# Optimization experiments

Measured on AMD Instinct MI355X. Metric: run time of the kernel, lower is better.

## Reference

```python
import jax, jax.numpy as jnp
import numpy as np

EPS = 1e-12  # tf.nn.l2_normalize epsilon


def setup_inputs() -> dict:
    key = jax.random.key(0)
    k1, k2, k3 = jax.random.split(key, 3)
    T, NC, FW = 16384, 2048, 100
    x = jax.random.normal(k1, (T, NC), dtype=jnp.float32)
    weights = jax.random.normal(k2, (FW, NC), dtype=jnp.float32)
    biases = jax.random.normal(k3, (1, NC), dtype=jnp.float32)
    return {"x": x, "weights": weights, "biases": biases}


def reference(x, weights, biases):
    # x: [T, NC] (batch_size is the time axis), weights: [FW, NC], biases: [1, NC]
    FW, NC = weights.shape
    # pos_constraint then L2-normalize each filter along the lag axis
    w = jnp.maximum(weights, 0.0)
    w = w * jax.lax.rsqrt(jnp.maximum(jnp.sum(w * w, axis=0, keepdims=True), EPS))
    # The original pads the filter with FW trailing zeros and runs a SAME conv2d
    # over a [NC, T, 1, 1] input, then takes diag_part to recover the per-channel
    # result. With kernel size 2*FW, SAME pads (FW-1) above / FW below; the FW
    # trailing zero taps never contribute, so this equals a cross-correlation
    # with left padding FW-1: out[t, c] = sum_k w[k, c] * x[t + k - (FW-1), c].
    xT = x.T[None]                 # [1, NC, T]
    kern = w.T[:, None, :]         # [NC, 1, FW] depthwise kernel (OIH)
    pre = jax.lax.conv_general_dilated(
        xT, kern,
        window_strides=(1,),
        padding=[(FW - 1, 0)],
        dimension_numbers=("NCH", "OIH", "NCH"),
        feature_group_count=NC,
    )                              # [1, NC, T]
    pre = pre[0].T + biases        # [T, NC]
    return pre  # activation_func='lin' -> identity
```

## Files before the change

### kernel.cpp

```cpp
#include <hip/hip_runtime.h>


#define T_TOT 16384
#define NCH   2048
#define FW    100
#define CB    32
#define TB    128
#define NTHR  256
#define TTH   16
#define ROWL  292
#define WROW  108
#define NSEG  12
#define NCHUNK_TOT (T_TOT / TB)

#define KC_PHASE(PH, NS) do {                                                   \
    int ro_ = tk & 255;                                                         \
    float4 n0_ = *(const float4*)(rrow + ro_);                                  \
    float4 n1_ = *(const float4*)(rrow + ro_ + 4);                              \
    float4 w0_ = *(const float4*)(wp);                                          \
    float4 w1_ = *(const float4*)(wp + 4);                                      \
    float wk_[8];                                                               \
    wk_[0]=w0_.x; wk_[1]=w0_.y; wk_[2]=w0_.z; wk_[3]=w0_.w;                     \
    wk_[4]=w1_.x; wk_[5]=w1_.y; wk_[6]=w1_.z; wk_[7]=w1_.w;                     \
    xw[(NS)+0]=n0_.x; xw[(NS)+1]=n0_.y; xw[(NS)+2]=n0_.z; xw[(NS)+3]=n0_.w;     \
    xw[(NS)+4]=n1_.x; xw[(NS)+5]=n1_.y; xw[(NS)+6]=n1_.z; xw[(NS)+7]=n1_.w;     \
    _Pragma("unroll")                                                           \
    for (int u_ = 0; u_ < 8; ++u_) {                                            \
      _Pragma("unroll")                                                         \
      for (int i_ = 0; i_ < 16; ++i_)                                           \
        acc[i_] = fmaf(wk_[u_], xw[((PH) + u_ + i_) % 24], acc[i_]);            \
    }                                                                           \
    tk += 8; wp += 8;                                                           \
} while (0)

__global__ __launch_bounds__(NTHR)
void catent_fir(const float* __restrict__ x,
                const float* __restrict__ wraw,
                const float* __restrict__ bias,
                float* __restrict__ out) {
    __shared__ float ring[CB * ROWL];
    __shared__ float wl[CB * WROW];
    __shared__ float scl[CB];

    const int tid   = threadIdx.x;
    const int cgrp  = blockIdx.x & 63;
    const int sidx  = blockIdx.x >> 6;
    const int cbase = cgrp * CB;

    const int ch0 = (sidx * NCHUNK_TOT) / NSEG;
    const int ch1 = ((sidx + 1) * NCHUNK_TOT) / NSEG;
    const int tseg0 = ch0 * TB;

    const int c = tid & 31;
    const int g = tid >> 5;

    for (int i = tid; i < FW * CB; i += NTHR) {
        int k = i >> 5, cc = i & 31;
        wl[cc * WROW + k + 1] = fmaxf(wraw[(size_t)k * NCH + cbase + cc], 0.0f);
    }
    if (tid < CB) {
        wl[tid * WROW + 0] = 0.0f;
        for (int j = FW + 1; j < WROW; ++j) wl[tid * WROW + j] = 0.0f;
    }
    __syncthreads();
    if (tid < CB) {
        float s = 0.0f;
        #pragma unroll 4
        for (int k = 1; k <= FW; ++k) { float v = wl[tid * WROW + k]; s = fmaf(v, v, s); }
        scl[tid] = rsqrtf(fmaxf(s, 1e-12f));
    }
    __syncthreads();
    for (int i = tid; i < FW * CB; i += NTHR) {
        int k = i >> 5, cc = i & 31;
        wl[cc * WROW + k + 1] *= scl[cc];
    }

    {
        float* rw = &ring[c * ROWL];
        for (int p = 0; p < 2; ++p) {
            int tbase = tseg0 - TB + p * TB + g * 16;
            float v[16];
            #pragma unroll
            for (int j = 0; j < 16; ++j) {
                int t = tbase + j;
                v[j] = (t >= 0) ? x[(size_t)t * NCH + cbase + c] : 0.0f;
            }
            int rm = tbase & 255;
            #pragma unroll
            for (int q = 0; q < 4; ++q)
                *(float4*)(rw + rm + q * 4) = make_float4(v[q*4], v[q*4+1], v[q*4+2], v[q*4+3]);
            if (rm < 32) {
                #pragma unroll
                for (int q = 0; q < 4; ++q)
                    *(float4*)(rw + 256 + rm + q * 4) = make_float4(v[q*4], v[q*4+1], v[q*4+2], v[q*4+3]);
            }
        }
    }
    __syncthreads();

    const float biasr = bias[cbase + c];
    const float* rrow = &ring[c * ROWL];
    const float* wrow = &wl[c * WROW];
    float* rwr = &ring[c * ROWL];

    for (int ch = ch0; ch < ch1; ++ch) {
        const int t0 = ch * TB;
        const bool do_stage = (ch + 1 < ch1);

        float stv[16];
        if (do_stage) {
            const size_t gb = (size_t)(t0 + TB + g * 16) * NCH + cbase + c;
            #pragma unroll
            for (int j = 0; j < 16; ++j) stv[j] = x[gb + (size_t)j * NCH];
        }

        float acc[16];
        #pragma unroll
        for (int i = 0; i < 16; ++i) acc[i] = biasr;

        float xw[24];
        const int base0 = t0 + g * 16 - 100;

        {
            int ro = base0 & 255;
            #pragma unroll
            for (int q = 0; q < 6; ++q) {
                float4 v = *(const float4*)(rrow + ro + q * 4);
                xw[q*4+0] = v.x; xw[q*4+1] = v.y; xw[q*4+2] = v.z; xw[q*4+3] = v.w;
            }
            float4 w0 = *(const float4*)(wrow);
            float4 w1 = *(const float4*)(wrow + 4);
            float wk[8];
            wk[0]=w0.x; wk[1]=w0.y; wk[2]=w0.z; wk[3]=w0.w;
            wk[4]=w1.x; wk[5]=w1.y; wk[6]=w1.z; wk[7]=w1.w;
            #pragma unroll
            for (int u = 0; u < 8; ++u) {
                #pragma unroll
                for (int i = 0; i < 16; ++i)
                    acc[i] = fmaf(wk[u], xw[(u + i) % 24], acc[i]);
            }
        }

        int tk = base0 + 24;
        const float* wp = wrow + 8;
        #pragma unroll 1
        for (int m = 0; m < 4; ++m) {
            KC_PHASE(8, 0);
            KC_PHASE(16, 8);
            KC_PHASE(0, 16);
        }

        __syncthreads();

        if (do_stage) {
            int rm = (t0 + TB + g * 16) & 255;
            #pragma unroll
            for (int q = 0; q < 4; ++q)
                *(float4*)(rwr + rm + q * 4) = make_float4(stv[q*4], stv[q*4+1], stv[q*4+2], stv[q*4+3]);
            if (rm < 32) {
                #pragma unroll
                for (int q = 0; q < 4; ++q)
                    *(float4*)(rwr + 256 + rm + q * 4) = make_float4(stv[q*4], stv[q*4+1], stv[q*4+2], stv[q*4+3]);
            }
        }
        __syncthreads();

        {
            size_t ob = (size_t)(t0 + g * 16) * NCH + cbase + c;
            #pragma unroll
            for (int i = 0; i < 16; ++i) out[ob + (size_t)i * NCH] = acc[i];
        }
    }
}

extern "C" void kernel_launch(void* const* d_in, const int* in_sizes, int n_in,
                              void* d_out, int out_size, void* d_ws, size_t ws_size,
                              hipStream_t stream) {
    const float* x    = (const float*)d_in[0];
    const float* wraw = (const float*)d_in[1];
    const float* bias = (const float*)d_in[2];
    float* out = (float*)d_out;

    dim3 grid(64 * NSEG);
    dim3 block(NTHR);
    catent_fir<<<grid, block, 0, stream>>>(x, wraw, bias, out);
}
```

Baseline: 111.6 us.

## Hold normalized FIR weights in registers and fully unroll tap loop

Each thread now loads its channel's 100 filter taps straight from global memory into a 104-entry register array, normalizes them there, and drops the shared-memory weight table. The tap loop is fully unrolled so weights are indexed statically and no LDS weight loads are needed. The time segmentation changes from 12 to 8 segments per channel group, and launch bounds now request 2 blocks per SIMD-level occupancy. This trades shared-memory traffic for much higher register pressure, which risks lower occupancy or spills, and fewer blocks means less parallelism.

```diff
diff --git a/kernel.cpp b/kernel.cpp
--- a/kernel.cpp
+++ b/kernel.cpp
@@ -7,72 +7,57 @@
 #define CB    32
 #define TB    128
 #define NTHR  256
-#define TTH   16
 #define ROWL  292
-#define WROW  108
-#define NSEG  12
-#define NCHUNK_TOT (T_TOT / TB)
+#define NSEG  8
+#define NCHUNK (T_TOT / TB / NSEG)
 
-#define KC_PHASE(PH, NS) do {                                                   \
-    int ro_ = tk & 255;                                                         \
+#define KC_STEP(KI, PH, NS) do {                                                \
+    int ro_ = (base0 + (KI)*8 + 16) & 255;                                      \
     float4 n0_ = *(const float4*)(rrow + ro_);                                  \
     float4 n1_ = *(const float4*)(rrow + ro_ + 4);                              \
-    float4 w0_ = *(const float4*)(wp);                                          \
-    float4 w1_ = *(const float4*)(wp + 4);                                      \
-    float wk_[8];                                                               \
-    wk_[0]=w0_.x; wk_[1]=w0_.y; wk_[2]=w0_.z; wk_[3]=w0_.w;                     \
-    wk_[4]=w1_.x; wk_[5]=w1_.y; wk_[6]=w1_.z; wk_[7]=w1_.w;                     \
     xw[(NS)+0]=n0_.x; xw[(NS)+1]=n0_.y; xw[(NS)+2]=n0_.z; xw[(NS)+3]=n0_.w;     \
     xw[(NS)+4]=n1_.x; xw[(NS)+5]=n1_.y; xw[(NS)+6]=n1_.z; xw[(NS)+7]=n1_.w;     \
     _Pragma("unroll")                                                           \
     for (int u_ = 0; u_ < 8; ++u_) {                                            \
       _Pragma("unroll")                                                         \
       for (int i_ = 0; i_ < 16; ++i_)                                           \
-        acc[i_] = fmaf(wk_[u_], xw[((PH) + u_ + i_) % 24], acc[i_]);            \
+        acc[i_] = fmaf(wreg[(KI)*8 + u_], xw[((PH) + u_ + i_) % 24], acc[i_]);  \
     }                                                                           \
-    tk += 8; wp += 8;                                                           \
 } while (0)
 
-__global__ __launch_bounds__(NTHR)
+__global__ __launch_bounds__(NTHR, 2)
 void catent_fir(const float* __restrict__ x,
                 const float* __restrict__ wraw,
                 const float* __restrict__ bias,
                 float* __restrict__ out) {
-    __shared__ float ring[CB * ROWL];
-    __shared__ float wl[CB * WROW];
-    __shared__ float scl[CB];
+    __shared__ __align__(16) float ring[CB * ROWL];
 
     const int tid   = threadIdx.x;
     const int cgrp  = blockIdx.x & 63;
     const int sidx  = blockIdx.x >> 6;
     const int cbase = cgrp * CB;
 
-    const int ch0 = (sidx * NCHUNK_TOT) / NSEG;
-    const int ch1 = ((sidx + 1) * NCHUNK_TOT) / NSEG;
+    const int ch0 = sidx * NCHUNK;
     const int tseg0 = ch0 * TB;
 
     const int c = tid & 31;
     const int g = tid >> 5;
 
-    for (int i = tid; i < FW * CB; i += NTHR) {
-        int k = i >> 5, cc = i & 31;
-        wl[cc * WROW + k + 1] = fmaxf(wraw[(size_t)k * NCH + cbase + cc], 0.0f);
-    }
-    if (tid < CB) {
-        wl[tid * WROW + 0] = 0.0f;
-        for (int j = FW + 1; j < WROW; ++j) wl[tid * WROW + j] = 0.0f;
-    }
-    __syncthreads();
-    if (tid < CB) {
+    float wreg[104];
+    {
+        const float* wcol = wraw + cbase + c;
         float s = 0.0f;
-        #pragma unroll 4
-        for (int k = 1; k <= FW; ++k) { float v = wl[tid * WROW + k]; s = fmaf(v, v, s); }
-        scl[tid] = rsqrtf(fmaxf(s, 1e-12f));
-    }
-    __syncthreads();
-    for (int i = tid; i < FW * CB; i += NTHR) {
-        int k = i >> 5, cc = i & 31;
-        wl[cc * WROW + k + 1] *= scl[cc];
+        wreg[0] = 0.0f;
+        #pragma unroll
+        for (int j = 1; j <= FW; ++j) {
+            float v = fmaxf(wcol[(size_t)(j - 1) * NCH], 0.0f);
+            wreg[j] = v;
+            s = fmaf(v, v, s);
+        }
+        wreg[101] = 0.0f; wreg[102] = 0.0f; wreg[103] = 0.0f;
+        float scl = rsqrtf(fmaxf(s, 1e-12f));
+        #pragma unroll
+        for (int j = 1; j <= FW; ++j) wreg[j] *= scl;
     }
 
     {
@@ -100,12 +85,11 @@
 
     const float biasr = bias[cbase + c];
     const float* rrow = &ring[c * ROWL];
-    const float* wrow = &wl[c * WROW];
     float* rwr = &ring[c * ROWL];
 
-    for (int ch = ch0; ch < ch1; ++ch) {
+    for (int ch = ch0; ch < ch0 + NCHUNK; ++ch) {
         const int t0 = ch * TB;
-        const bool do_stage = (ch + 1 < ch1);
+        const bool do_stage = (ch + 1 < ch0 + NCHUNK);
 
         float stv[16];
         if (do_stage) {
@@ -128,27 +112,26 @@
                 float4 v = *(const float4*)(rrow + ro + q * 4);
                 xw[q*4+0] = v.x; xw[q*4+1] = v.y; xw[q*4+2] = v.z; xw[q*4+3] = v.w;
             }
-            float4 w0 = *(const float4*)(wrow);
-            float4 w1 = *(const float4*)(wrow + 4);
-            float wk[8];
-            wk[0]=w0.x; wk[1]=w0.y; wk[2]=w0.z; wk[3]=w0.w;
-            wk[4]=w1.x; wk[5]=w1.y; wk[6]=w1.z; wk[7]=w1.w;
             #pragma unroll
             for (int u = 0; u < 8; ++u) {
                 #pragma unroll
                 for (int i = 0; i < 16; ++i)
-                    acc[i] = fmaf(wk[u], xw[(u + i) % 24], acc[i]);
+                    acc[i] = fmaf(wreg[u], xw[(u + i) % 24], acc[i]);
             }
         }
 
-        int tk = base0 + 24;
-        const float* wp = wrow + 8;
-        #pragma unroll 1
-        for (int m = 0; m < 4; ++m) {
-            KC_PHASE(8, 0);
-            KC_PHASE(16, 8);
-            KC_PHASE(0, 16);
-        }
+        KC_STEP(1,  8, 0);
+        KC_STEP(2, 16, 8);
+        KC_STEP(3,  0, 16);
+        KC_STEP(4,  8, 0);
+        KC_STEP(5, 16, 8);
+        KC_STEP(6,  0, 16);
+        KC_STEP(7,  8, 0);
+        KC_STEP(8, 16, 8);
+        KC_STEP(9,  0, 16);
+        KC_STEP(10, 8, 0);
+        KC_STEP(11,16, 8);
+        KC_STEP(12, 0, 16);
 
         __syncthreads();
 
```

Measured after the change: 107.1 us. -4.1%, faster.
